# Performance work log

Measured on AMD Instinct MI355X. Metric: run time of the kernel, lower is better.

## Reference

```python
import jax, jax.numpy as jnp
import numpy as np

N_NODES = 100000
N_EDGES = 3200000
F_IN = 128
HID = 16
N_CLASSES = 40


def setup_inputs() -> dict:
    key = jax.random.key(0)
    ks = jax.random.split(key, 9)
    x = jax.random.normal(ks[0], (N_NODES, F_IN), dtype=jnp.float32)
    edge_index = jax.random.randint(ks[1], (2, N_EDGES), 0, N_NODES, dtype=jnp.int64)
    edge_attr = jax.random.uniform(ks[2], (N_EDGES, 1), dtype=jnp.float32)
    # SplineConv params: weight [kernel_size^dim=2, in, out], root lin, bias
    s1 = 1.0 / np.sqrt(F_IN)
    W1 = jax.random.uniform(ks[3], (2, F_IN, HID), dtype=jnp.float32, minval=-s1, maxval=s1)
    root1 = jax.random.uniform(ks[4], (F_IN, HID), dtype=jnp.float32, minval=-s1, maxval=s1)
    bias1 = jnp.zeros((HID,), dtype=jnp.float32)
    s2 = 1.0 / np.sqrt(HID)
    W2 = jax.random.uniform(ks[5], (2, HID, N_CLASSES), dtype=jnp.float32, minval=-s2, maxval=s2)
    root2 = jax.random.uniform(ks[6], (HID, N_CLASSES), dtype=jnp.float32, minval=-s2, maxval=s2)
    bias2 = jnp.zeros((N_CLASSES,), dtype=jnp.float32)
    return {"x": x, "edge_index": edge_index, "edge_attr": edge_attr,
            "W1": W1, "root1": root1, "bias1": bias1,
            "W2": W2, "root2": root2, "bias2": bias2}


def _spline_conv(x, src, dst, b0, b1, W, root, bias, n_nodes):
    # dim=1, kernel_size=2, degree=1 open B-spline: basis = (1-u, u) on weight[0], weight[1].
    # Transform all nodes once (dense GEMM), then per-edge blend + gather + scatter-mean.
    X0 = x @ W[0]                                   # [N, out]
    X1 = x @ W[1]                                   # [N, out]
    m = b0[:, None] * X0[src] + b1[:, None] * X1[src]  # [E, out] per-edge messages
    agg = jax.ops.segment_sum(m, dst, num_segments=n_nodes)
    cnt = jax.ops.segment_sum(jnp.ones_like(dst, dtype=x.dtype), dst, num_segments=n_nodes)
    agg = agg / jnp.maximum(cnt, 1.0)[:, None]      # aggr='mean'
    return agg + x @ root + bias                    # root_weight + bias


def reference(x, edge_index, edge_attr, W1, root1, bias1, W2, root2, bias2):
    src, dst = edge_index[0], edge_index[1]
    u = edge_attr[:, 0]
    b0, b1 = 1.0 - u, u
    n = x.shape[0]
    # dropout is identity in eval mode (training=False)
    h = jax.nn.elu(_spline_conv(x, src, dst, b0, b1, W1, root1, bias1, n))
    out = _spline_conv(h, src, dst, b0, b1, W2, root2, bias2, n)
    return jax.nn.log_softmax(out, axis=1)
```

## Files before the change

### kernel.cpp

```cpp
#include <hip/hip_runtime.h>
#include <cstddef>

#define NN 100000
#define NE 3200000
#define FIN 128
#define HID 16
#define NC 40
#define NBUK 196
#define BUKCAP 20480
#define CHUNK 4096
#define NBLK_BKT ((NE + CHUNK - 1) / CHUNK)
#define NWAVE_G1 (NN / 16)
#define NBLK_G1 ((NWAVE_G1 + 3) / 4)

typedef __attribute__((ext_vector_type(8))) short bf16x8;
typedef __attribute__((ext_vector_type(4))) float f32x4;
typedef __attribute__((ext_vector_type(2))) float f32x2;


__device__ __forceinline__ unsigned bf16rne(float f) {
  unsigned u = __float_as_uint(f);
  return (u + 0x7fffu + ((u >> 16) & 1u)) >> 16;
}
__device__ __forceinline__ unsigned bfpack(float lo, float hi) {
  return bf16rne(lo) | (bf16rne(hi) << 16);
}
__device__ __forceinline__ float bflo(unsigned w) { return __uint_as_float(w << 16); }
__device__ __forceinline__ float bfhi(unsigned w) { return __uint_as_float(w & 0xffff0000u); }

__device__ __forceinline__ unsigned short fp8pack2(float a, float b) {
#if __has_builtin(__builtin_amdgcn_cvt_pk_fp8_f32)
  return (unsigned short)__builtin_amdgcn_cvt_pk_fp8_f32(a, b, 0, false);
#else
  auto enc1 = [](float f) -> unsigned {
    float y = f * 0x1p-120f;
    unsigned bb = __float_as_uint(y);
    unsigned s = (bb >> 24) & 0x80u;
    unsigned m = bb & 0x7fffffffu;
    const unsigned maxb = (15u << 23) | (6u << 20);
    m = m + 0x7ffffu + ((m >> 20) & 1u);
    if (m > maxb) m = maxb;
    return s | (m >> 20);
  };
  return (unsigned short)(enc1(a) | (enc1(b) << 8));
#endif
}
template <bool HI>
__device__ __forceinline__ f32x2 fp8unpack2(unsigned w) {
#if __has_builtin(__builtin_amdgcn_cvt_pk_f32_fp8)
  return __builtin_amdgcn_cvt_pk_f32_fp8((int)w, HI);
#else
  unsigned w2 = HI ? (w >> 16) : w;
  auto dec1 = [](unsigned b) -> float {
    unsigned f = ((b & 0x80u) << 24) | ((b & 0x7fu) << 20);
    return __uint_as_float(f) * 0x1p120f;
  };
  f32x2 r;
  r.x = dec1(w2 & 0xffu);
  r.y = dec1((w2 >> 8) & 0xffu);
  return r;
#endif
}

__global__ __launch_bounds__(256) void k_init(int* __restrict__ bcur) {
  int t = threadIdx.x;
  if (t < NBUK) bcur[t] = t * BUKCAP;
}

__global__ __launch_bounds__(256) void k_pre(const float* __restrict__ x,
    const float* __restrict__ W1, const float* __restrict__ root1,
    const float* __restrict__ bias1,
    unsigned char* __restrict__ XD8, float* __restrict__ XR,
    const int* __restrict__ ei, const float* __restrict__ ea,
    int* __restrict__ bcur, unsigned* __restrict__ bx) {
  __shared__ int lh[NBUK];
  __shared__ int lbase[NBUK];
  __shared__ int gb[NBUK];
  __shared__ int scn[256];
  __shared__ unsigned meta[CHUNK];
  __shared__ unsigned char sbkt[CHUNK];
  int t = threadIdx.x;
  if (blockIdx.x >= NBLK_G1) {
    for (int i = t; i < NBUK; i += 256) lh[i] = 0;
    __syncthreads();
    int base = (blockIdx.x - NBLK_G1) * CHUNK;
    int rk[16], bk[16];
    unsigned mt[16];
#pragma unroll
    for (int i = 0; i < 16; ++i) {
      int e = base + i * 256 + t;
      if (e < NE) {
        int d = ei[NE + e], sv = ei[e];
        int b = d >> 9;
        rk[i] = atomicAdd(&lh[b], 1);
        bk[i] = b;
        unsigned u6 = (unsigned)__float2int_rn(ea[e] * 63.0f);
        mt[i] = (u6 << 26) | ((unsigned)(d & 511) << 17) | (unsigned)sv;
      } else bk[i] = -1;
    }
    __syncthreads();
    int v = (t < NBUK) ? lh[t] : 0;
    scn[t] = v;
    __syncthreads();
    for (int st = 1; st < 256; st <<= 1) {
      int tmp = (t >= st) ? scn[t - st] : 0;
      __syncthreads();
      scn[t] += tmp;
      __syncthreads();
    }
    if (t < NBUK) lbase[t] = scn[t] - v;
    int total = scn[255];
    __syncthreads();
    if (t < NBUK && lh[t] > 0) gb[t] = atomicAdd(&bcur[t], lh[t]);
    __syncthreads();
#pragma unroll
    for (int i = 0; i < 16; ++i) {
      if (bk[i] >= 0) {
        int p = lbase[bk[i]] + rk[i];
        meta[p] = mt[i];
        sbkt[p] = (unsigned char)bk[i];
      }
    }
    __syncthreads();
    for (int s = t; s < total; s += 256) {
      int b = sbkt[s];
      bx[gb[b] + (s - lbase[b])] = meta[s];
    }
    return;
  }
  int l = t & 63;
  int wv = (blockIdx.x * 256 + t) >> 6;
  int nb = wv * 16;
  if (nb >= NN) return;
  int j16 = l & 15, kg = l >> 4;

  bf16x8 bfrag[3][4];
  const float* wsrc0 = W1;
  const float* wsrc1 = W1 + 2048;
  const float* wsrc2 = root1;
#pragma unroll
  for (int kk = 0; kk < 4; ++kk) {
    int krow = kk * 32 + kg * 8;
#pragma unroll
    for (int b = 0; b < 8; ++b) {
      int o = (krow + b) * 16 + j16;
      bfrag[0][kk][b] = (short)bf16rne(wsrc0[o]);
      bfrag[1][kk][b] = (short)bf16rne(wsrc1[o]);
      bfrag[2][kk][b] = (short)bf16rne(wsrc2[o]);
    }
  }

  f32x4 acc0 = {0.f, 0.f, 0.f, 0.f};
  f32x4 acc1 = {0.f, 0.f, 0.f, 0.f};
  f32x4 acc2 = {0.f, 0.f, 0.f, 0.f};
  const float* xrow = x + (size_t)(nb + j16) * FIN + kg * 8;
#pragma unroll
  for (int kk = 0; kk < 4; ++kk) {
    float4 xa = *(const float4*)(xrow + kk * 32);
    float4 xb = *(const float4*)(xrow + kk * 32 + 4);
    bf16x8 a;
    a[0] = (short)bf16rne(xa.x); a[1] = (short)bf16rne(xa.y);
    a[2] = (short)bf16rne(xa.z); a[3] = (short)bf16rne(xa.w);
    a[4] = (short)bf16rne(xb.x); a[5] = (short)bf16rne(xb.y);
    a[6] = (short)bf16rne(xb.z); a[7] = (short)bf16rne(xb.w);
    acc0 = __builtin_amdgcn_mfma_f32_16x16x32_bf16(a, bfrag[0][kk], acc0, 0, 0, 0);
    acc1 = __builtin_amdgcn_mfma_f32_16x16x32_bf16(a, bfrag[1][kk], acc1, 0, 0, 0);
    acc2 = __builtin_amdgcn_mfma_f32_16x16x32_bf16(a, bfrag[2][kk], acc2, 0, 0, 0);
  }

  float bb = bias1[j16];
#pragma unroll
  for (int r = 0; r < 4; ++r) {
    int n = nb + kg * 4 + r;
    *(unsigned short*)(XD8 + (size_t)n * 32 + j16 * 2) =
        fp8pack2(acc0[r], acc1[r] - acc0[r]);
    XR[(size_t)n * HID + j16] = acc2[r] + bb;
  }
}

__global__ __launch_bounds__(1024) void k_csr(const unsigned* __restrict__ bx,
    const int* __restrict__ bcur, int2* __restrict__ off2,
    unsigned* __restrict__ sedge) {
  __shared__ int cnt[512];
  __shared__ int scn[512];
  __shared__ int cur[512];
  int b = blockIdx.x, t = threadIdx.x;
  int s0 = b * BUKCAP, s1 = bcur[b];
  if (t < 512) cnt[t] = 0;
  __syncthreads();
  for (int i = s0 + t; i < s1; i += 1024)
    atomicAdd(&cnt[(bx[i] >> 17) & 511], 1);
  __syncthreads();
  int v = (t < 512) ? cnt[t] : 0;
  if (t < 512) scn[t] = v;
  __syncthreads();
  for (int st = 1; st < 512; st <<= 1) {
    int tmp = (t < 512 && t >= st) ? scn[t - st] : 0;
    __syncthreads();
    if (t < 512) scn[t] += tmp;
    __syncthreads();
  }
  if (t < 512) {
    int n = (b << 9) + t;
    if (n < NN) off2[n] = make_int2(s0 + scn[t] - v, s0 + scn[t]);
    cur[t] = s0 + scn[t] - v;
  }
  __syncthreads();
  for (int i = s0 + t; i < s1; i += 1024) {
    unsigned r = bx[i];
    int pos = atomicAdd(&cur[(r >> 17) & 511], 1);
    sedge[pos] = r;
  }
}


__global__ __launch_bounds__(256) void k_pull1(const int2* __restrict__ off2,
    const unsigned* __restrict__ sedge, const unsigned char* __restrict__ XD8,
    const float* __restrict__ XR, unsigned* __restrict__ Hb,
    unsigned* __restrict__ H8) {
  int tid = blockIdx.x * 256 + threadIdx.x;
  int n = tid >> 3, ch = tid & 1, q = (tid >> 1) & 3;
  if (n >= NN) return;
  int2 o = off2[n];
  int start = o.x, end = o.y, len = end - start;
  int lo = start + (len * q) / 4;
  int hi = start + (len * (q + 1)) / 4;
  float acc[8] = {0.f, 0.f, 0.f, 0.f, 0.f, 0.f, 0.f, 0.f};
  int i = lo;
  for (; i + 4 <= hi; i += 4) {
    unsigned se[4];
    uint4 w[4];
#pragma unroll
    for (int e = 0; e < 4; ++e) se[e] = sedge[i + e];
#pragma unroll
    for (int e = 0; e < 4; ++e)
      w[e] = *(const uint4*)(XD8 + (size_t)(se[e] & 131071u) * 32 + ch * 16);
#pragma unroll
    for (int e = 0; e < 4; ++e) {
      float u = (float)(se[e] >> 26) * (1.0f / 63.0f);
      f32x2 p;
      p = fp8unpack2<false>(w[e].x); acc[0] += p.x + u * p.y;
      p = fp8unpack2<true>(w[e].x);  acc[1] += p.x + u * p.y;
      p = fp8unpack2<false>(w[e].y); acc[2] += p.x + u * p.y;
      p = fp8unpack2<true>(w[e].y);  acc[3] += p.x + u * p.y;
      p = fp8unpack2<false>(w[e].z); acc[4] += p.x + u * p.y;
      p = fp8unpack2<true>(w[e].z);  acc[5] += p.x + u * p.y;
      p = fp8unpack2<false>(w[e].w); acc[6] += p.x + u * p.y;
      p = fp8unpack2<true>(w[e].w);  acc[7] += p.x + u * p.y;
    }
  }
  for (; i < hi; ++i) {
    unsigned se = sedge[i];
    float u = (float)(se >> 26) * (1.0f / 63.0f);
    uint4 w = *(const uint4*)(XD8 + (size_t)(se & 131071u) * 32 + ch * 16);
    f32x2 p;
    p = fp8unpack2<false>(w.x); acc[0] += p.x + u * p.y;
    p = fp8unpack2<true>(w.x);  acc[1] += p.x + u * p.y;
    p = fp8unpack2<false>(w.y); acc[2] += p.x + u * p.y;
    p = fp8unpack2<true>(w.y);  acc[3] += p.x + u * p.y;
    p = fp8unpack2<false>(w.z); acc[4] += p.x + u * p.y;
    p = fp8unpack2<true>(w.z);  acc[5] += p.x + u * p.y;
    p = fp8unpack2<false>(w.w); acc[6] += p.x + u * p.y;
    p = fp8unpack2<true>(w.w);  acc[7] += p.x + u * p.y;
  }
#pragma unroll
  for (int k = 0; k < 8; ++k) {
    acc[k] += __shfl_xor(acc[k], 2);
    acc[k] += __shfl_xor(acc[k], 4);
  }
  if (q) return;
  float ic = 1.0f / fmaxf((float)len, 1.0f);
  const float* xr = XR + (size_t)n * HID + ch * 8;
  float4 r0 = *(const float4*)xr;
  float4 r1 = *(const float4*)(xr + 4);
  float h[8];
  h[0] = acc[0] * ic + r0.x;
  h[1] = acc[1] * ic + r0.y;
  h[2] = acc[2] * ic + r0.z;
  h[3] = acc[3] * ic + r0.w;
  h[4] = acc[4] * ic + r1.x;
  h[5] = acc[5] * ic + r1.y;
  h[6] = acc[6] * ic + r1.z;
  h[7] = acc[7] * ic + r1.w;
#pragma unroll
  for (int k = 0; k < 8; ++k) h[k] = h[k] > 0.f ? h[k] : expm1f(h[k]);
  uint4 hw;
  hw.x = bfpack(h[0], h[1]);
  hw.y = bfpack(h[2], h[3]);
  hw.z = bfpack(h[4], h[5]);
  hw.w = bfpack(h[6], h[7]);
  *(uint4*)(Hb + (size_t)n * 8 + ch * 4) = hw;
  uint2 h8w;
  h8w.x = (unsigned)fp8pack2(h[0], h[1]) | ((unsigned)fp8pack2(h[2], h[3]) << 16);
  h8w.y = (unsigned)fp8pack2(h[4], h[5]) | ((unsigned)fp8pack2(h[6], h[7]) << 16);
  *(uint2*)(H8 + (size_t)n * 4 + ch * 2) = h8w;
}

__global__ __launch_bounds__(256) void k_pull2f(const int2* __restrict__ off2,
    const unsigned* __restrict__ sedge, const unsigned* __restrict__ H8,
    const unsigned* __restrict__ Hb, const float* __restrict__ W2,
    const float* __restrict__ root2, const float* __restrict__ bias2,
    float* __restrict__ out) {
  __shared__ float a0s[32 * 16];
  __shared__ float a1s[32 * 16];
  __shared__ float ics[32];
  int t = threadIdx.x;
  int nb = blockIdx.x * 32;
  int ln0 = t >> 3, ch = t & 1, q = (t >> 1) & 3;
  int n = nb + ln0;
  float ss[8] = {0.f, 0.f, 0.f, 0.f, 0.f, 0.f, 0.f, 0.f};
  float a1[8] = {0.f, 0.f, 0.f, 0.f, 0.f, 0.f, 0.f, 0.f};
  int len = 0;
  if (n < NN) {
    int2 o = off2[n];
    int start = o.x, end = o.y;
    len = end - start;
    int lo = start + (len * q) / 4;
    int hi = start + (len * (q + 1)) / 4;
    int i = lo;
    for (; i + 4 <= hi; i += 4) {
      unsigned se[4];
      uint2 w[4];
#pragma unroll
      for (int e = 0; e < 4; ++e) se[e] = sedge[i + e];
#pragma unroll
      for (int e = 0; e < 4; ++e)
        w[e] = *(const uint2*)(H8 + (size_t)(se[e] & 131071u) * 4 + ch * 2);
#pragma unroll
      for (int e = 0; e < 4; ++e) {
        float u = (float)(se[e] >> 26) * (1.0f / 63.0f);
        f32x2 p;
        p = fp8unpack2<false>(w[e].x); ss[0] += p.x; a1[0] += u * p.x; ss[1] += p.y; a1[1] += u * p.y;
        p = fp8unpack2<true>(w[e].x);  ss[2] += p.x; a1[2] += u * p.x; ss[3] += p.y; a1[3] += u * p.y;
        p = fp8unpack2<false>(w[e].y); ss[4] += p.x; a1[4] += u * p.x; ss[5] += p.y; a1[5] += u * p.y;
        p = fp8unpack2<true>(w[e].y);  ss[6] += p.x; a1[6] += u * p.x; ss[7] += p.y; a1[7] += u * p.y;
      }
    }
    for (; i < hi; ++i) {
      unsigned se = sedge[i];
      float u = (float)(se >> 26) * (1.0f / 63.0f);
      uint2 w = *(const uint2*)(H8 + (size_t)(se & 131071u) * 4 + ch * 2);
      f32x2 p;
      p = fp8unpack2<false>(w.x); ss[0] += p.x; a1[0] += u * p.x; ss[1] += p.y; a1[1] += u * p.y;
      p = fp8unpack2<true>(w.x);  ss[2] += p.x; a1[2] += u * p.x; ss[3] += p.y; a1[3] += u * p.y;
      p = fp8unpack2<false>(w.y); ss[4] += p.x; a1[4] += u * p.x; ss[5] += p.y; a1[5] += u * p.y;
      p = fp8unpack2<true>(w.y);  ss[6] += p.x; a1[6] += u * p.x; ss[7] += p.y; a1[7] += u * p.y;
    }
  }
#pragma unroll
  for (int k = 0; k < 8; ++k) {
    ss[k] += __shfl_xor(ss[k], 2);
    ss[k] += __shfl_xor(ss[k], 4);
    a1[k] += __shfl_xor(a1[k], 2);
    a1[k] += __shfl_xor(a1[k], 4);
  }
  if (q == 0 && n < NN) {
#pragma unroll
    for (int k = 0; k < 8; ++k) {
      a0s[ln0 * 16 + ch * 8 + k] = ss[k] - a1[k];
      a1s[ln0 * 16 + ch * 8 + k] = a1[k];
    }
    if (ch == 0) ics[ln0] = 1.0f / fmaxf((float)len, 1.0f);
  }
  __syncthreads();

  int l = t & 63;
  int wv = t >> 6;
  int j = (l < NC) ? l : 0;
  float w0r[HID], w1r[HID], rr[HID];
#pragma unroll
  for (int k = 0; k < HID; ++k) {
    w0r[k] = W2[k * NC + j];
    w1r[k] = W2[HID * NC + k * NC + j];
    rr[k]  = root2[k * NC + j];
  }
  float b2 = bias2[j];
#pragma unroll 1
  for (int qq = 0; qq < 8; ++qq) {
    int ln = wv * 8 + qq;
    int nn = nb + ln;
    if (nn >= NN) break;
    nn = __builtin_amdgcn_readfirstlane(nn);
    float ic = ics[ln];
    const unsigned* hp = Hb + (size_t)nn * 8;
    float accm = 0.f, accr = 0.f;
#pragma unroll
    for (int k = 0; k < HID; ++k) {
      accm += a0s[ln * 16 + k] * w0r[k];
      accm += a1s[ln * 16 + k] * w1r[k];
      unsigned hw = hp[k >> 1];
      float hk = (k & 1) ? bfhi(hw) : bflo(hw);
      accr += hk * rr[k];
    }
    float logit = accm * ic + accr + b2;
    float mx = (l < NC) ? logit : -INFINITY;
#pragma unroll
    for (int o = 32; o >= 1; o >>= 1) mx = fmaxf(mx, __shfl_xor(mx, o));
    float p = (l < NC) ? __expf(logit - mx) : 0.f;
    float sm = p;
#pragma unroll
    for (int o = 32; o >= 1; o >>= 1) sm += __shfl_xor(sm, o);
    if (l < NC) out[(size_t)nn * NC + l] = logit - mx - __logf(sm);
  }
}

extern "C" void kernel_launch(void* const* d_in, const int* in_sizes, int n_in,
                              void* d_out, int out_size, void* d_ws, size_t ws_size,
                              hipStream_t stream) {
  const float* x     = (const float*)d_in[0];
  const int*   ei    = (const int*)d_in[1];
  const float* ea    = (const float*)d_in[2];
  const float* W1    = (const float*)d_in[3];
  const float* root1 = (const float*)d_in[4];
  const float* bias1 = (const float*)d_in[5];
  const float* W2    = (const float*)d_in[6];
  const float* root2 = (const float*)d_in[7];
  const float* bias2 = (const float*)d_in[8];
  float* out = (float*)d_out;
  char* base = (char*)d_ws;

  unsigned char* XD8   = (unsigned char*)base;
  float*         XR    = (float*)(base + 3200000);
  unsigned*      Hb    = (unsigned*)(base + 9600000);
  unsigned*      H8    = (unsigned*)(base + 12800000);
  unsigned*      bx    = (unsigned*)(base + 14400000);
  unsigned*      sedge = (unsigned*)(base + 14400000 + (size_t)NBUK * BUKCAP * 4);
  int2*          off2  = (int2*)(base + 14400000 + 2 * (size_t)NBUK * BUKCAP * 4);
  int*           bcur  = (int*)(off2 + NN);

  k_init<<<1, 256, 0, stream>>>(bcur);
  k_pre<<<NBLK_G1 + NBLK_BKT, 256, 0, stream>>>(x, W1, root1, bias1, XD8, XR,
                                                ei, ea, bcur, bx);
  k_csr<<<NBUK, 1024, 0, stream>>>(bx, bcur, off2, sedge);
  k_pull1<<<(NN * 8 + 255) / 256, 256, 0, stream>>>(off2, sedge, XD8, XR, Hb, H8);
  k_pull2f<<<(NN + 31) / 32, 256, 0, stream>>>(off2, sedge, H8, Hb, W2, root2, bias2, out);
}
```

Baseline: 146.9 us.

## Stage CSR scatter in LDS and widen layer-2 gather to full rows

The CSR build kernel now keeps each thread's bucket records in registers together with the rank returned by the counting atomic. It places them into an LDS staging buffer at their final offsets and then writes sedge out contiguously, which removes the second global read pass, the second atomic pass and the scattered global writes. The layer-2 pull kernel now has each thread load a full 16-byte FP8 row instead of half a row, so 4 threads cover a node and a block handles 64 nodes. The costs are 80KB of LDS per CSR block, higher register use for 20 records per thread and 16-wide accumulators, and a silent clamp of bucket size to BUKCAP.

```diff
diff --git a/kernel.cpp b/kernel.cpp
--- a/kernel.cpp
+++ b/kernel.cpp
@@ -12,6 +12,7 @@
 #define NBLK_BKT ((NE + CHUNK - 1) / CHUNK)
 #define NWAVE_G1 (NN / 16)
 #define NBLK_G1 ((NWAVE_G1 + 3) / 4)
+#define CSR_MAXPT 20
 
 typedef __attribute__((ext_vector_type(8))) short bf16x8;
 typedef __attribute__((ext_vector_type(4))) float f32x4;
@@ -183,13 +184,24 @@
     unsigned* __restrict__ sedge) {
   __shared__ int cnt[512];
   __shared__ int scn[512];
-  __shared__ int cur[512];
+  __shared__ unsigned stage[BUKCAP];
   int b = blockIdx.x, t = threadIdx.x;
-  int s0 = b * BUKCAP, s1 = bcur[b];
+  int s0 = b * BUKCAP;
+  int m = bcur[b] - s0;
+  if (m > BUKCAP) m = BUKCAP;
   if (t < 512) cnt[t] = 0;
   __syncthreads();
-  for (int i = s0 + t; i < s1; i += 1024)
-    atomicAdd(&cnt[(bx[i] >> 17) & 511], 1);
+  unsigned rec[CSR_MAXPT];
+  int rnk[CSR_MAXPT];
+#pragma unroll
+  for (int e = 0; e < CSR_MAXPT; ++e) {
+    int i = t + e * 1024;
+    if (i < m) {
+      unsigned r = bx[s0 + i];
+      rec[e] = r;
+      rnk[e] = atomicAdd(&cnt[(r >> 17) & 511], 1);
+    }
+  }
   __syncthreads();
   int v = (t < 512) ? cnt[t] : 0;
   if (t < 512) scn[t] = v;
@@ -203,14 +215,20 @@
   if (t < 512) {
     int n = (b << 9) + t;
     if (n < NN) off2[n] = make_int2(s0 + scn[t] - v, s0 + scn[t]);
-    cur[t] = s0 + scn[t] - v;
-  }
-  __syncthreads();
-  for (int i = s0 + t; i < s1; i += 1024) {
-    unsigned r = bx[i];
-    int pos = atomicAdd(&cur[(r >> 17) & 511], 1);
-    sedge[pos] = r;
-  }
+  }
+  __syncthreads();
+#pragma unroll
+  for (int e = 0; e < CSR_MAXPT; ++e) {
+    int i = t + e * 1024;
+    if (i < m) {
+      unsigned r = rec[e];
+      int local = (r >> 17) & 511;
+      stage[scn[local] - cnt[local] + rnk[e]] = r;
+    }
+  }
+  __syncthreads();
+  for (int i = t; i < m; i += 1024)
+    sedge[s0 + i] = stage[i];
 }
 
 
@@ -301,66 +319,75 @@
     const unsigned* __restrict__ Hb, const float* __restrict__ W2,
     const float* __restrict__ root2, const float* __restrict__ bias2,
     float* __restrict__ out) {
-  __shared__ float a0s[32 * 16];
-  __shared__ float a1s[32 * 16];
-  __shared__ float ics[32];
+  __shared__ float a0s[64 * 16];
+  __shared__ float a1s[64 * 16];
+  __shared__ float ics[64];
   int t = threadIdx.x;
-  int nb = blockIdx.x * 32;
-  int ln0 = t >> 3, ch = t & 1, q = (t >> 1) & 3;
+  int nb = blockIdx.x * 64;
+  int ln0 = t >> 2, q = t & 3;
   int n = nb + ln0;
-  float ss[8] = {0.f, 0.f, 0.f, 0.f, 0.f, 0.f, 0.f, 0.f};
-  float a1[8] = {0.f, 0.f, 0.f, 0.f, 0.f, 0.f, 0.f, 0.f};
+  float ss[16], a1[16];
+#pragma unroll
+  for (int k = 0; k < 16; ++k) { ss[k] = 0.f; a1[k] = 0.f; }
   int len = 0;
   if (n < NN) {
     int2 o = off2[n];
-    int start = o.x, end = o.y;
-    len = end - start;
+    int start = o.x;
+    len = o.y - o.x;
     int lo = start + (len * q) / 4;
     int hi = start + (len * (q + 1)) / 4;
     int i = lo;
     for (; i + 4 <= hi; i += 4) {
       unsigned se[4];
-      uint2 w[4];
+      uint4 w[4];
 #pragma unroll
       for (int e = 0; e < 4; ++e) se[e] = sedge[i + e];
 #pragma unroll
       for (int e = 0; e < 4; ++e)
-        w[e] = *(const uint2*)(H8 + (size_t)(se[e] & 131071u) * 4 + ch * 2);
+        w[e] = *(const uint4*)(H8 + (size_t)(se[e] & 131071u) * 4);
 #pragma unroll
       for (int e = 0; e < 4; ++e) {
         float u = (float)(se[e] >> 26) * (1.0f / 63.0f);
         f32x2 p;
-        p = fp8unpack2<false>(w[e].x); ss[0] += p.x; a1[0] += u * p.x; ss[1] += p.y; a1[1] += u * p.y;
-        p = fp8unpack2<true>(w[e].x);  ss[2] += p.x; a1[2] += u * p.x; ss[3] += p.y; a1[3] += u * p.y;
-        p = fp8unpack2<false>(w[e].y); ss[4] += p.x; a1[4] += u * p.x; ss[5] += p.y; a1[5] += u * p.y;
-        p = fp8unpack2<true>(w[e].y);  ss[6] += p.x; a1[6] += u * p.x; ss[7] += p.y; a1[7] += u * p.y;
+        p = fp8unpack2<false>(w[e].x); ss[0]+=p.x; a1[0]+=u*p.x; ss[1]+=p.y; a1[1]+=u*p.y;
+        p = fp8unpack2<true>(w[e].x);  ss[2]+=p.x; a1[2]+=u*p.x; ss[3]+=p.y; a1[3]+=u*p.y;
+        p = fp8unpack2<false>(w[e].y); ss[4]+=p.x; a1[4]+=u*p.x; ss[5]+=p.y; a1[5]+=u*p.y;
+        p = fp8unpack2<true>(w[e].y);  ss[6]+=p.x; a1[6]+=u*p.x; ss[7]+=p.y; a1[7]+=u*p.y;
+        p = fp8unpack2<false>(w[e].z); ss[8]+=p.x; a1[8]+=u*p.x; ss[9]+=p.y; a1[9]+=u*p.y;
+        p = fp8unpack2<true>(w[e].z);  ss[10]+=p.x; a1[10]+=u*p.x; ss[11]+=p.y; a1[11]+=u*p.y;
+        p = fp8unpack2<false>(w[e].w); ss[12]+=p.x; a1[12]+=u*p.x; ss[13]+=p.y; a1[13]+=u*p.y;
+        p = fp8unpack2<true>(w[e].w);  ss[14]+=p.x; a1[14]+=u*p.x; ss[15]+=p.y; a1[15]+=u*p.y;
       }
     }
     for (; i < hi; ++i) {
       unsigned se = sedge[i];
       float u = (float)(se >> 26) * (1.0f / 63.0f);
-      uint2 w = *(const uint2*)(H8 + (size_t)(se & 131071u) * 4 + ch * 2);
+      uint4 w = *(const uint4*)(H8 + (size_t)(se & 131071u) * 4);
       f32x2 p;
-      p = fp8unpack2<false>(w.x); ss[0] += p.x; a1[0] += u * p.x; ss[1] += p.y; a1[1] += u * p.y;
-      p = fp8unpack2<true>(w.x);  ss[2] += p.x; a1[2] += u * p.x; ss[3] += p.y; a1[3] += u * p.y;
-      p = fp8unpack2<false>(w.y); ss[4] += p.x; a1[4] += u * p.x; ss[5] += p.y; a1[5] += u * p.y;
-      p = fp8unpack2<true>(w.y);  ss[6] += p.x; a1[6] += u * p.x; ss[7] += p.y; a1[7] += u * p.y;
-    }
-  }
-#pragma unroll
-  for (int k = 0; k < 8; ++k) {
+      p = fp8unpack2<false>(w.x); ss[0]+=p.x; a1[0]+=u*p.x; ss[1]+=p.y; a1[1]+=u*p.y;
+      p = fp8unpack2<true>(w.x);  ss[2]+=p.x; a1[2]+=u*p.x; ss[3]+=p.y; a1[3]+=u*p.y;
+      p = fp8unpack2<false>(w.y); ss[4]+=p.x; a1[4]+=u*p.x; ss[5]+=p.y; a1[5]+=u*p.y;
+      p = fp8unpack2<true>(w.y);  ss[6]+=p.x; a1[6]+=u*p.x; ss[7]+=p.y; a1[7]+=u*p.y;
+      p = fp8unpack2<false>(w.z); ss[8]+=p.x; a1[8]+=u*p.x; ss[9]+=p.y; a1[9]+=u*p.y;
+      p = fp8unpack2<true>(w.z);  ss[10]+=p.x; a1[10]+=u*p.x; ss[11]+=p.y; a1[11]+=u*p.y;
+      p = fp8unpack2<false>(w.w); ss[12]+=p.x; a1[12]+=u*p.x; ss[13]+=p.y; a1[13]+=u*p.y;
+      p = fp8unpack2<true>(w.w);  ss[14]+=p.x; a1[14]+=u*p.x; ss[15]+=p.y; a1[15]+=u*p.y;
+    }
+  }
+#pragma unroll
+  for (int k = 0; k < 16; ++k) {
+    ss[k] += __shfl_xor(ss[k], 1);
     ss[k] += __shfl_xor(ss[k], 2);
-    ss[k] += __shfl_xor(ss[k], 4);
+    a1[k] += __shfl_xor(a1[k], 1);
     a1[k] += __shfl_xor(a1[k], 2);
-    a1[k] += __shfl_xor(a1[k], 4);
   }
   if (q == 0 && n < NN) {
 #pragma unroll
-    for (int k = 0; k < 8; ++k) {
-      a0s[ln0 * 16 + ch * 8 + k] = ss[k] - a1[k];
-      a1s[ln0 * 16 + ch * 8 + k] = a1[k];
-    }
-    if (ch == 0) ics[ln0] = 1.0f / fmaxf((float)len, 1.0f);
+    for (int k = 0; k < 16; ++k) {
+      a0s[ln0 * 16 + k] = ss[k] - a1[k];
+      a1s[ln0 * 16 + k] = a1[k];
+    }
+    ics[ln0] = 1.0f / fmaxf((float)len, 1.0f);
   }
   __syncthreads();
 
@@ -376,8 +403,8 @@
   }
   float b2 = bias2[j];
 #pragma unroll 1
-  for (int qq = 0; qq < 8; ++qq) {
-    int ln = wv * 8 + qq;
+  for (int qq = 0; qq < 16; ++qq) {
+    int ln = wv * 16 + qq;
     int nn = nb + ln;
     if (nn >= NN) break;
     nn = __builtin_amdgcn_readfirstlane(nn);
@@ -433,5 +460,5 @@
                                                 ei, ea, bcur, bx);
   k_csr<<<NBUK, 1024, 0, stream>>>(bx, bcur, off2, sedge);
   k_pull1<<<(NN * 8 + 255) / 256, 256, 0, stream>>>(off2, sedge, XD8, XR, Hb, H8);
-  k_pull2f<<<(NN + 31) / 32, 256, 0, stream>>>(off2, sedge, H8, Hb, W2, root2, bias2, out);
-}
+  k_pull2f<<<(NN + 63) / 64, 256, 0, stream>>>(off2, sedge, H8, Hb, W2, root2, bias2, out);
+}
```

After: 144.5 us. No clear change (-1.7%).
